# Optimization experiments

Measured on AMD Instinct MI355X. Metric: run time of the kernel, lower is better.

The kernel has to match this reference:

```python
import jax, jax.numpy as jnp
import numpy as np

VOCAB, D = 50000, 256
B, R, C, T = 4, 64, 64, 32


def setup_inputs() -> dict:
    key = jax.random.key(0)
    k1, k2, k3 = jax.random.split(key, 3)
    x = jax.random.randint(k1, (B, R, C, T), 0, VOCAB, dtype=jnp.int32)
    E = jax.random.normal(k2, (VOCAB, D), dtype=jnp.float32)
    W = jax.random.normal(k3, (D,), dtype=jnp.float32) * (1.0 / np.sqrt(D))
    b = jnp.zeros((1,), dtype=jnp.float32)
    return {"x": x, "E": E, "W": W, "b": b}


def reference(x, E, W, b):
    # Fused version of the per-cell Python loop:
    #   embed tokens, sum over token dim, (dropout = identity in eval), linear -> scalar per cell.
    emb_sum = E[x].sum(axis=3)                      # [B, R, C, D]
    scores = jnp.einsum("brcd,d->brc", emb_sum, W) + b[0]  # [B, R, C]
    return scores
```

## Files before the change

### kernel.cpp

```cpp
#include <hip/hip_runtime.h>

#define VOCAB_SZ 50000
#define EMB_D    256
#define N_CELLS  (4 * 64 * 64)
#define TOK_T    32

__global__ void __launch_bounds__(256)
vocab_dot_kernel(const float* __restrict__ E, const float* __restrict__ W,
                 float* __restrict__ s) {
    const int gtid = blockIdx.x * blockDim.x + threadIdx.x;
    const int row  = gtid >> 6;
    const int lane = threadIdx.x & 63;
    if (row >= VOCAB_SZ) return;

    const float4 e = *reinterpret_cast<const float4*>(E + (size_t)row * EMB_D + lane * 4);
    const float4 w = *reinterpret_cast<const float4*>(W + lane * 4);
    float p = e.x * w.x + e.y * w.y + e.z * w.z + e.w * w.w;

    #pragma unroll
    for (int off = 32; off > 0; off >>= 1)
        p += __shfl_xor(p, off);

    if (lane == 0) s[row] = p;
}

__global__ void __launch_bounds__(256)
cell_sum_kernel(const int* __restrict__ x, const float* __restrict__ s,
                const float* __restrict__ b, float* __restrict__ out) {
    const int cell = blockIdx.x * blockDim.x + threadIdx.x;
    if (cell >= N_CELLS) return;

    const int4* xp = reinterpret_cast<const int4*>(x + (size_t)cell * TOK_T);
    float acc = 0.0f;
    #pragma unroll
    for (int i = 0; i < TOK_T / 4; ++i) {
        const int4 v = xp[i];
        acc += s[v.x];
        acc += s[v.y];
        acc += s[v.z];
        acc += s[v.w];
    }
    out[cell] = acc + b[0];
}

extern "C" void kernel_launch(void* const* d_in, const int* in_sizes, int n_in,
                              void* d_out, int out_size, void* d_ws, size_t ws_size,
                              hipStream_t stream) {
    const int*   x = (const int*)d_in[0];
    const float* E = (const float*)d_in[1];
    const float* W = (const float*)d_in[2];
    const float* b = (const float*)d_in[3];
    float* out = (float*)d_out;
    float* s   = (float*)d_ws;

    {
        const int waves_per_block = 256 / 64;
        const int grid = (VOCAB_SZ + waves_per_block - 1) / waves_per_block;
        vocab_dot_kernel<<<grid, 256, 0, stream>>>(E, W, s);
    }

    {
        const int grid = (N_CELLS + 255) / 256;
        cell_sum_kernel<<<grid, 256, 0, stream>>>(x, s, b, out);
    }
}
```

Baseline: 96.53 us.

## Restructure vocab dot and cell sum kernels for coalesced, wider parallel work

The vocab projection kernel becomes a grid-stride loop with a fixed 1024-block grid. Each wave handles four rows at once using 16-lane subgroups. W is loaded once per thread, and a shorter 4-step shuffle reduction replaces the 6-step one. The cell-sum kernel spreads each cell across 8 threads, each reading one int4 of token ids with adjacent lanes at adjacent addresses, and combines them with a shuffle reduction. This is meant to fix the strided per-thread loads of x and to cut block-launch and reduction overhead, at the cost of eight times more threads in the cell-sum kernel.

Result: faster. 93.09 us (-3.6%).

```diff
diff --git a/kernel.cpp b/kernel.cpp
--- a/kernel.cpp
+++ b/kernel.cpp
@@ -8,39 +8,55 @@
 __global__ void __launch_bounds__(256)
 vocab_dot_kernel(const float* __restrict__ E, const float* __restrict__ W,
                  float* __restrict__ s) {
-    const int gtid = blockIdx.x * blockDim.x + threadIdx.x;
-    const int row  = gtid >> 6;
-    const int lane = threadIdx.x & 63;
-    if (row >= VOCAB_SZ) return;
+    const int tid    = blockIdx.x * blockDim.x + threadIdx.x;
+    const int wave   = tid >> 6;
+    const int lane   = threadIdx.x & 63;
+    const int sub    = lane & 15;
+    const int grp    = lane >> 4;
+    const int nwaves = (gridDim.x * blockDim.x) >> 6;
 
-    const float4 e = *reinterpret_cast<const float4*>(E + (size_t)row * EMB_D + lane * 4);
-    const float4 w = *reinterpret_cast<const float4*>(W + lane * 4);
-    float p = e.x * w.x + e.y * w.y + e.z * w.z + e.w * w.w;
+    const float4 w0 = *reinterpret_cast<const float4*>(W +   0 + sub * 4);
+    const float4 w1 = *reinterpret_cast<const float4*>(W +  64 + sub * 4);
+    const float4 w2 = *reinterpret_cast<const float4*>(W + 128 + sub * 4);
+    const float4 w3 = *reinterpret_cast<const float4*>(W + 192 + sub * 4);
 
-    #pragma unroll
-    for (int off = 32; off > 0; off >>= 1)
-        p += __shfl_xor(p, off);
+    const int ngroups = VOCAB_SZ / 4;
+    for (int g = wave; g < ngroups; g += nwaves) {
+        const int row = g * 4 + grp;
+        const float* er = E + (size_t)row * EMB_D;
+        const float4 e0 = *reinterpret_cast<const float4*>(er +   0 + sub * 4);
+        const float4 e1 = *reinterpret_cast<const float4*>(er +  64 + sub * 4);
+        const float4 e2 = *reinterpret_cast<const float4*>(er + 128 + sub * 4);
+        const float4 e3 = *reinterpret_cast<const float4*>(er + 192 + sub * 4);
 
-    if (lane == 0) s[row] = p;
+        float p = e0.x*w0.x + e0.y*w0.y + e0.z*w0.z + e0.w*w0.w;
+        p      += e1.x*w1.x + e1.y*w1.y + e1.z*w1.z + e1.w*w1.w;
+        p      += e2.x*w2.x + e2.y*w2.y + e2.z*w2.z + e2.w*w2.w;
+        p      += e3.x*w3.x + e3.y*w3.y + e3.z*w3.z + e3.w*w3.w;
+
+        p += __shfl_xor(p, 1);
+        p += __shfl_xor(p, 2);
+        p += __shfl_xor(p, 4);
+        p += __shfl_xor(p, 8);
+
+        if (sub == 0) s[row] = p;
+    }
 }
 
 __global__ void __launch_bounds__(256)
 cell_sum_kernel(const int* __restrict__ x, const float* __restrict__ s,
                 const float* __restrict__ b, float* __restrict__ out) {
-    const int cell = blockIdx.x * blockDim.x + threadIdx.x;
-    if (cell >= N_CELLS) return;
+    const int tid = blockIdx.x * blockDim.x + threadIdx.x;
+    if (tid >= N_CELLS * (TOK_T / 4)) return;
 
-    const int4* xp = reinterpret_cast<const int4*>(x + (size_t)cell * TOK_T);
-    float acc = 0.0f;
-    #pragma unroll
-    for (int i = 0; i < TOK_T / 4; ++i) {
-        const int4 v = xp[i];
-        acc += s[v.x];
-        acc += s[v.y];
-        acc += s[v.z];
-        acc += s[v.w];
-    }
-    out[cell] = acc + b[0];
+    const int4 v = reinterpret_cast<const int4*>(x)[tid];
+    float acc = s[v.x] + s[v.y] + s[v.z] + s[v.w];
+
+    acc += __shfl_xor(acc, 1);
+    acc += __shfl_xor(acc, 2);
+    acc += __shfl_xor(acc, 4);
+
+    if ((threadIdx.x & 7) == 0) out[tid >> 3] = acc + b[0];
 }
 
 extern "C" void kernel_launch(void* const* d_in, const int* in_sizes, int n_in,
@@ -53,14 +69,7 @@
     float* out = (float*)d_out;
     float* s   = (float*)d_ws;
 
-    {
-        const int waves_per_block = 256 / 64;
-        const int grid = (VOCAB_SZ + waves_per_block - 1) / waves_per_block;
-        vocab_dot_kernel<<<grid, 256, 0, stream>>>(E, W, s);
-    }
+    vocab_dot_kernel<<<1024, 256, 0, stream>>>(E, W, s);
 
-    {
-        const int grid = (N_CELLS + 255) / 256;
-        cell_sum_kernel<<<grid, 256, 0, stream>>>(x, s, b, out);
-    }
+    cell_sum_kernel<<<512, 256, 0, stream>>>(x, s, b, out);
 }
```
